# Optimization experiments

Hardware: AMD Instinct MI355X
Metric: run time of the kernel (lower is better)

Reference implementation:

```python
import jax, jax.numpy as jnp
import numpy as np

N_NODES = 100000
N_EDGES = 1600000
IN_FEATS = 128
HIDDEN = 150
NUM_OUT = 128


def setup_inputs() -> dict:
    key = jax.random.key(0)
    ks = jax.random.split(key, 9)
    x = jax.random.normal(ks[0], (N_NODES, IN_FEATS), dtype=jnp.float32)
    src = jax.random.randint(ks[1], (N_EDGES,), 0, N_NODES, dtype=jnp.int32)
    dst = jax.random.randint(ks[2], (N_EDGES,), 0, N_NODES, dtype=jnp.int32)
    def lin(k, fan_in, fan_out):
        bound = 1.0 / np.sqrt(fan_in)
        return jax.random.uniform(k, (fan_in, fan_out), jnp.float32, -bound, bound)
    W_self1 = lin(ks[3], IN_FEATS, HIDDEN)
    W_neigh1 = lin(ks[4], IN_FEATS, HIDDEN)
    b1 = jnp.zeros((HIDDEN,), jnp.float32)
    W_self2 = lin(ks[5], HIDDEN, NUM_OUT)
    W_neigh2 = lin(ks[6], HIDDEN, NUM_OUT)
    b2 = jnp.zeros((NUM_OUT,), jnp.float32)
    return {"x": x, "src": src, "dst": dst,
            "W_self1": W_self1, "W_neigh1": W_neigh1, "b1": b1,
            "W_self2": W_self2, "W_neigh2": W_neigh2, "b2": b2}


def _mean_agg(h, src, dst, deg_inv):
    # segment-mean of source features onto destination nodes; isolated nodes -> 0
    summed = jax.ops.segment_sum(h[src], dst, num_segments=N_NODES)
    return summed * deg_inv[:, None]


def _sage_conv(h, src, dst, deg_inv, W_self, W_neigh, b):
    h_neigh = _mean_agg(h, src, dst, deg_inv)
    return h @ W_self + h_neigh @ W_neigh + b


def reference(x, src, dst, W_self1, W_neigh1, b1, W_self2, W_neigh2, b2):
    deg = jax.ops.segment_sum(jnp.ones((src.shape[0],), x.dtype), dst,
                              num_segments=N_NODES)
    deg_inv = jnp.where(deg > 0, 1.0 / jnp.maximum(deg, 1.0), 0.0)
    h = _sage_conv(x, src, dst, deg_inv, W_self1, W_neigh1, b1)
    h = jax.nn.relu(h)
    h = _sage_conv(h, src, dst, deg_inv, W_self2, W_neigh2, b2)
    return h
```

## Files before the change

### kernel.cpp

```cpp
#include <hip/hip_runtime.h>

#define NN 100000
#define NE 1600000
#define INF 128
#define HID 150
#define NOUT 128

#define NBK 196
#define WGS 400
#define EPW 4000
#define CNTL (NBK * WGS)
#define CAP2 10240

typedef __attribute__((ext_vector_type(8))) short bf16x8;
typedef __attribute__((ext_vector_type(8))) unsigned short u16x8;
typedef __attribute__((ext_vector_type(4))) float f32x4;

__device__ inline unsigned short f2bf(float f) {
    unsigned int u = __float_as_uint(f);
    u += 0x7fffu + ((u >> 16) & 1u);
    return (unsigned short)(u >> 16);
}
__device__ inline float bflo(unsigned int t) { return __uint_as_float(t << 16); }
__device__ inline float bfhi(unsigned int t) { return __uint_as_float(t & 0xffff0000u); }


__global__ __launch_bounds__(256) void sort1(const int* __restrict__ src,
                                             const int* __restrict__ dst,
                                             unsigned int* __restrict__ chunkw,
                                             int* __restrict__ cntm,
                                             int* __restrict__ exm) {
    __shared__ int hist[NBK];
    __shared__ int off[NBK];
    __shared__ int s[256];
    __shared__ unsigned int buf[EPW];
    int w = blockIdx.x, tid = threadIdx.x;
    int e0 = w * EPW;
    for (int i = tid; i < NBK; i += 256) hist[i] = 0;
    __syncthreads();
    for (int i = tid; i < EPW; i += 256) atomicAdd(&hist[dst[e0 + i] >> 9], 1);
    __syncthreads();
    int v = (tid < NBK) ? hist[tid] : 0;
    s[tid] = v;
    __syncthreads();
    for (int o = 1; o < 256; o <<= 1) {
        int t = (tid >= o) ? s[tid - o] : 0;
        __syncthreads();
        s[tid] += t;
        __syncthreads();
    }
    if (tid < NBK) {
        int ex = s[tid] - v;
        off[tid] = ex;
        cntm[tid * WGS + w] = v;
        exm[tid * WGS + w] = ex;
    }
    __syncthreads();
    for (int i = tid; i < EPW; i += 256) {
        int d = dst[e0 + i];
        int b = d >> 9;
        int p = atomicAdd(&off[b], 1);
        buf[p] = (unsigned int)src[e0 + i] | ((unsigned int)(d & 511) << 17);
    }
    __syncthreads();
    for (int i = tid; i < EPW; i += 256) chunkw[e0 + i] = buf[i];
}

__global__ void scanA(const int* __restrict__ in, int* __restrict__ excl,
                      int* __restrict__ blk_sums, int L) {
    __shared__ int s[256];
    int i = blockIdx.x * 256 + threadIdx.x;
    int d = (i < L) ? in[i] : 0;
    s[threadIdx.x] = d;
    __syncthreads();
    for (int o = 1; o < 256; o <<= 1) {
        int t = (threadIdx.x >= o) ? s[threadIdx.x - o] : 0;
        __syncthreads();
        s[threadIdx.x] += t;
        __syncthreads();
    }
    int incl = s[threadIdx.x];
    if (i < L) excl[i] = incl - d;
    if (threadIdx.x == 255) blk_sums[blockIdx.x] = incl;
}

__global__ void scanB(int* __restrict__ blk_sums, int nb) {
    __shared__ int s[512];
    int t = threadIdx.x;
    int v = (t < nb) ? blk_sums[t] : 0;
    s[t] = v;
    __syncthreads();
    for (int o = 1; o < 512; o <<= 1) {
        int u = (t >= o) ? s[t - o] : 0;
        __syncthreads();
        s[t] += u;
        __syncthreads();
    }
    if (t < nb) blk_sums[t] = s[t] - v;
}

__global__ void scanC(int* __restrict__ excl, const int* __restrict__ blk_sums, int L) {
    int i = blockIdx.x * 256 + threadIdx.x;
    if (i < L) excl[i] += blk_sums[blockIdx.x];
}

__global__ __launch_bounds__(256) void buildcsr(const unsigned int* __restrict__ chunkw,
                                                const int* __restrict__ offm,
                                                const int* __restrict__ exm,
                                                int* __restrict__ csr_ptr,
                                                float* __restrict__ deg_inv,
                                                int* __restrict__ csr_src) {
    __shared__ int offrow[WGS + 1];
    __shared__ int exrow[WGS];
    __shared__ int cnt[512];
    __shared__ int excl[512];
    __shared__ int off[512];
    __shared__ int s[256];
    __shared__ int span[CAP2];
    int b = blockIdx.x, tid = threadIdx.x;
    for (int i = tid; i < WGS; i += 256) {
        offrow[i] = offm[b * WGS + i];
        exrow[i] = exm[b * WGS + i];
    }
    if (tid == 0) offrow[WGS] = (b == NBK - 1) ? NE : offm[(b + 1) * WGS];
    for (int i = tid; i < 512; i += 256) cnt[i] = 0;
    __syncthreads();
    int base = offrow[0];
    int n = offrow[WGS] - base;
    if (n > CAP2) n = CAP2;
    for (int i = tid; i < n; i += 256) {
        int gi = base + i;
        int lo = 0, hi = WGS;
        while (hi - lo > 1) {
            int mid = (lo + hi) >> 1;
            if (offrow[mid] <= gi) lo = mid; else hi = mid;
        }
        unsigned int wd = chunkw[lo * EPW + exrow[lo] + (gi - offrow[lo])];
        atomicAdd(&cnt[wd >> 17], 1);
        csr_src[gi] = (int)wd;
    }
    __syncthreads();
    int a0 = cnt[2 * tid], a1 = cnt[2 * tid + 1];
    int ps = a0 + a1;
    s[tid] = ps;
    __syncthreads();
    for (int o = 1; o < 256; o <<= 1) {
        int t = (tid >= o) ? s[tid - o] : 0;
        __syncthreads();
        s[tid] += t;
        __syncthreads();
    }
    int ex = s[tid] - ps;
    excl[2 * tid] = ex;
    excl[2 * tid + 1] = ex + a0;
    off[2 * tid] = ex;
    off[2 * tid + 1] = ex + a0;
    __syncthreads();
    for (int l = tid; l < 512; l += 256) {
        int g = b * 512 + l;
        if (g < NN) {
            csr_ptr[g] = base + excl[l];
            int d = cnt[l];
            deg_inv[g] = d > 0 ? 1.0f / (float)d : 0.0f;
        }
    }
    if (b == NBK - 1 && tid == 0) csr_ptr[NN] = NE;
    for (int i = tid; i < n; i += 256) {
        unsigned int wd = (unsigned int)csr_src[base + i];
        int l = wd >> 17;
        int p = atomicAdd(&off[l], 1);
        span[p] = (int)(wd & 0x1FFFFu);
    }
    __syncthreads();
    for (int i = tid; i < n; i += 256) csr_src[base + i] = span[i];
}


__global__ void cast_bf16(const float* __restrict__ in, unsigned short* __restrict__ outb,
                          int n8) {
    int i = blockIdx.x * 256 + threadIdx.x;
    if (i >= n8) return;
    const float4* p = (const float4*)in;
    float4 v0 = p[(size_t)i * 2];
    float4 v1 = p[(size_t)i * 2 + 1];
    u16x8 o = {f2bf(v0.x), f2bf(v0.y), f2bf(v0.z), f2bf(v0.w),
               f2bf(v1.x), f2bf(v1.y), f2bf(v1.z), f2bf(v1.w)};
    ((u16x8*)outb)[i] = o;
}

__global__ void pack_weights(const float* __restrict__ Ws1, const float* __restrict__ Wn1,
                             const float* __restrict__ b1,
                             const float* __restrict__ Ws2, const float* __restrict__ Wn2,
                             unsigned short* __restrict__ W1t, unsigned short* __restrict__ W2t,
                             float* __restrict__ b1p) {
    int id = blockIdx.x * 256 + threadIdx.x;
    if (id < 160 * 256) {
        int n = id >> 8, k = id & 255;
        float v = 0.f;
        if (n < HID) v = (k < 128) ? Ws1[k * HID + n] : Wn1[(k - 128) * HID + n];
        W1t[id] = f2bf(v);
    } else if (id < 160 * 256 + 256 * 160) {
        int id2 = id - 160 * 256;
        int n = id2 / 160, k = id2 - n * 160;
        float v = 0.f;
        if (k < HID) v = (n < 128) ? Ws2[k * 128 + n] : Wn2[k * 128 + (n - 128)];
        W2t[id2] = f2bf(v);
    } else if (id < 160 * 256 + 256 * 160 + 160) {
        int n = id - (160 * 256 + 256 * 160);
        b1p[n] = (n < HID) ? b1[n] : 0.f;
    }
}


#define AGG_ACC(t)                    \
    acc0 += bflo(t.x); acc1 += bfhi(t.x); \
    acc2 += bflo(t.y); acc3 += bfhi(t.y); \
    acc4 += bflo(t.z); acc5 += bfhi(t.z); \
    acc6 += bflo(t.w); acc7 += bfhi(t.w);

#define AGG_Q_BODY(SRCPTR)                                                  \
    int wid = threadIdx.x >> 6;                                             \
    int lane = threadIdx.x & 63;                                            \
    int v = blockIdx.x * 4 + wid;                                           \
    int start = csr_ptr[v], end = csr_ptr[v + 1];                           \
    int rg = lane >> 4, ch = lane & 15;                                     \
    const uint4* f4 = (const uint4*)(SRCPTR);                               \
    float acc0 = 0.f, acc1 = 0.f, acc2 = 0.f, acc3 = 0.f;                   \
    float acc4 = 0.f, acc5 = 0.f, acc6 = 0.f, acc7 = 0.f;                   \
    int e = start;                                                          \
    for (; e + 16 <= end; e += 16) {                                        \
        int s0 = csr_src[e + rg];                                           \
        int s1 = csr_src[e + 4 + rg];                                       \
        int s2 = csr_src[e + 8 + rg];                                       \
        int s3 = csr_src[e + 12 + rg];                                      \
        uint4 t0 = f4[(size_t)s0 * 16 + ch];                                \
        uint4 t1 = f4[(size_t)s1 * 16 + ch];                                \
        uint4 t2 = f4[(size_t)s2 * 16 + ch];                                \
        uint4 t3 = f4[(size_t)s3 * 16 + ch];                                \
        AGG_ACC(t0); AGG_ACC(t1); AGG_ACC(t2); AGG_ACC(t3);                 \
    }                                                                       \
    for (; e + 4 <= end; e += 4) {                                          \
        int s0 = csr_src[e + rg];                                           \
        uint4 t0 = f4[(size_t)s0 * 16 + ch];                                \
        AGG_ACC(t0);                                                        \
    }                                                                       \
    int rem = end - e;                                                      \
    if (rem > 0) {                                                          \
        int s0 = csr_src[(rg < rem) ? (e + rg) : e];                        \
        uint4 t = f4[(size_t)s0 * 16 + ch];                                 \
        float wt = (rg < rem) ? 1.f : 0.f;                                  \
        acc0 += wt * bflo(t.x); acc1 += wt * bfhi(t.x);                     \
        acc2 += wt * bflo(t.y); acc3 += wt * bfhi(t.y);                     \
        acc4 += wt * bflo(t.z); acc5 += wt * bfhi(t.z);                     \
        acc6 += wt * bflo(t.w); acc7 += wt * bfhi(t.w);                     \
    }                                                                       \
    acc0 += __shfl_xor(acc0, 32); acc1 += __shfl_xor(acc1, 32);             \
    acc2 += __shfl_xor(acc2, 32); acc3 += __shfl_xor(acc3, 32);             \
    acc4 += __shfl_xor(acc4, 32); acc5 += __shfl_xor(acc5, 32);             \
    acc6 += __shfl_xor(acc6, 32); acc7 += __shfl_xor(acc7, 32);             \
    acc0 += __shfl_xor(acc0, 16); acc1 += __shfl_xor(acc1, 16);             \
    acc2 += __shfl_xor(acc2, 16); acc3 += __shfl_xor(acc3, 16);             \
    acc4 += __shfl_xor(acc4, 16); acc5 += __shfl_xor(acc5, 16);             \
    acc6 += __shfl_xor(acc6, 16); acc7 += __shfl_xor(acc7, 16);

__global__ __launch_bounds__(256) void agg_mean_q(
    const unsigned short* __restrict__ featb, const int* __restrict__ csr_ptr,
    const float* __restrict__ deg_inv, const int* __restrict__ csr_src,
    unsigned short* __restrict__ outb) {
    AGG_Q_BODY(featb)
    if (lane < 16) {
        float di = deg_inv[v];
        u16x8 o = {f2bf(acc0 * di), f2bf(acc1 * di), f2bf(acc2 * di), f2bf(acc3 * di),
                   f2bf(acc4 * di), f2bf(acc5 * di), f2bf(acc6 * di), f2bf(acc7 * di)};
        ((u16x8*)outb)[(size_t)v * 16 + ch] = o;
    }
}

__global__ __launch_bounds__(256) void agg_add_q(
    const unsigned short* __restrict__ zb, const int* __restrict__ csr_ptr,
    const float* __restrict__ deg_inv, const int* __restrict__ csr_src,
    float* __restrict__ out) {
    AGG_Q_BODY(zb)
    if (lane < 16) {
        float di = deg_inv[v];
        float4* o4 = (float4*)out;
        size_t base = (size_t)v * 32 + ch * 2;
        float4 c0 = o4[base];
        float4 c1 = o4[base + 1];
        c0.x += acc0 * di; c0.y += acc1 * di; c0.z += acc2 * di; c0.w += acc3 * di;
        c1.x += acc4 * di; c1.y += acc5 * di; c1.z += acc6 * di; c1.w += acc7 * di;
        o4[base] = c0;
        o4[base + 1] = c1;
    }
}


__global__ __launch_bounds__(256) void gemm1_mfma(
    const unsigned short* __restrict__ xb, const unsigned short* __restrict__ aggb,
    const unsigned short* __restrict__ W1t, const float* __restrict__ b1p,
    unsigned short* __restrict__ h1b) {
    __shared__ __align__(16) unsigned short A_lds[128][40];
    __shared__ __align__(16) unsigned short B_lds[160][40];
    int tid = threadIdx.x;
    int m0 = blockIdx.x * 128;
    int w = tid >> 6, lane = tid & 63;
    int lrow = lane & 15, quad = lane >> 4;
    int wr = (w & 1) * 64;
    int wc = (w >> 1) * 80;
    f32x4 acc[4][5];
    #pragma unroll
    for (int r = 0; r < 4; r++)
        #pragma unroll
        for (int c = 0; c < 5; c++) acc[r][c] = (f32x4){0.f, 0.f, 0.f, 0.f};

    for (int k0 = 0; k0 < 256; k0 += 32) {
        __syncthreads();
        #pragma unroll
        for (int i = 0; i < 2; i++) {
            int idx = tid + i * 256;
            int row = idx >> 2, ch = idx & 3;
            int gm = m0 + row, gk = k0 + ch * 8;
            u16x8 val = {0, 0, 0, 0, 0, 0, 0, 0};
            if (gm < NN) {
                const unsigned short* sp = (gk < 128)
                    ? (xb + (size_t)gm * 128 + gk)
                    : (aggb + (size_t)gm * 128 + (gk - 128));
                val = *(const u16x8*)sp;
            }
            *(u16x8*)&A_lds[row][ch * 8] = val;
        }
        #pragma unroll
        for (int i = 0; i < 3; i++) {
            int idx = tid + i * 256;
            if (idx < 640) {
                int n = idx >> 2, ch = idx & 3;
                u16x8 val = *(const u16x8*)(W1t + (size_t)n * 256 + k0 + ch * 8);
                *(u16x8*)&B_lds[n][ch * 8] = val;
            }
        }
        __syncthreads();
        bf16x8 a[4], b[5];
        #pragma unroll
        for (int r = 0; r < 4; r++)
            a[r] = *(const bf16x8*)&A_lds[wr + r * 16 + lrow][quad * 8];
        #pragma unroll
        for (int c = 0; c < 5; c++)
            b[c] = *(const bf16x8*)&B_lds[wc + c * 16 + lrow][quad * 8];
        #pragma unroll
        for (int r = 0; r < 4; r++)
            #pragma unroll
            for (int c = 0; c < 5; c++)
                acc[r][c] = __builtin_amdgcn_mfma_f32_16x16x32_bf16(a[r], b[c], acc[r][c], 0, 0, 0);
    }
    #pragma unroll
    for (int r = 0; r < 4; r++) {
        #pragma unroll
        for (int rr = 0; rr < 4; rr++) {
            int gm = m0 + wr + r * 16 + quad * 4 + rr;
            if (gm < NN) {
                #pragma unroll
                for (int c = 0; c < 5; c++) {
                    int gn = wc + c * 16 + lrow;
                    float val = acc[r][c][rr] + b1p[gn];
                    val = val > 0.f ? val : 0.f;
                    h1b[(size_t)gm * 160 + gn] = f2bf(val);
                }
            }
        }
    }
}

__global__ __launch_bounds__(256) void gemm2_mfma(
    const unsigned short* __restrict__ h1b, const unsigned short* __restrict__ W2t,
    const float* __restrict__ b2, float* __restrict__ out,
    unsigned short* __restrict__ zb) {
    __shared__ __align__(16) unsigned short A_lds[128][40];
    __shared__ __align__(16) unsigned short B_lds[128][40];
    int tid = threadIdx.x;
    int m0 = blockIdx.x * 128;
    int n0 = blockIdx.y * 128;
    int w = tid >> 6, lane = tid & 63;
    int lrow = lane & 15, quad = lane >> 4;
    int wr = (w & 1) * 64;
    int wc = (w >> 1) * 64;
    f32x4 acc[4][4];
    #pragma unroll
    for (int r = 0; r < 4; r++)
        #pragma unroll
        for (int c = 0; c < 4; c++) acc[r][c] = (f32x4){0.f, 0.f, 0.f, 0.f};

    for (int k0 = 0; k0 < 160; k0 += 32) {
        __syncthreads();
        #pragma unroll
        for (int i = 0; i < 2; i++) {
            int idx = tid + i * 256;
            int row = idx >> 2, ch = idx & 3;
            int gm = m0 + row;
            u16x8 val = {0, 0, 0, 0, 0, 0, 0, 0};
            if (gm < NN) val = *(const u16x8*)(h1b + (size_t)gm * 160 + k0 + ch * 8);
            *(u16x8*)&A_lds[row][ch * 8] = val;
        }
        #pragma unroll
        for (int i = 0; i < 2; i++) {
            int idx = tid + i * 256;
            int n = idx >> 2, ch = idx & 3;
            u16x8 val = *(const u16x8*)(W2t + (size_t)(n0 + n) * 160 + k0 + ch * 8);
            *(u16x8*)&B_lds[n][ch * 8] = val;
        }
        __syncthreads();
        bf16x8 a[4], b[4];
        #pragma unroll
        for (int r = 0; r < 4; r++)
            a[r] = *(const bf16x8*)&A_lds[wr + r * 16 + lrow][quad * 8];
        #pragma unroll
        for (int c = 0; c < 4; c++)
            b[c] = *(const bf16x8*)&B_lds[wc + c * 16 + lrow][quad * 8];
        #pragma unroll
        for (int r = 0; r < 4; r++)
            #pragma unroll
            for (int c = 0; c < 4; c++)
                acc[r][c] = __builtin_amdgcn_mfma_f32_16x16x32_bf16(a[r], b[c], acc[r][c], 0, 0, 0);
    }
    #pragma unroll
    for (int r = 0; r < 4; r++) {
        #pragma unroll
        for (int rr = 0; rr < 4; rr++) {
            int gm = m0 + wr + r * 16 + quad * 4 + rr;
            if (gm < NN) {
                #pragma unroll
                for (int c = 0; c < 4; c++) {
                    int gn = wc + c * 16 + lrow;
                    float val = acc[r][c][rr];
                    if (n0 == 0) {
                        out[(size_t)gm * 128 + gn] = val + b2[gn];
                    } else {
                        zb[(size_t)gm * 128 + gn] = f2bf(val);
                    }
                }
            }
        }
    }
}


extern "C" void kernel_launch(void* const* d_in, const int* in_sizes, int n_in,
                              void* d_out, int out_size, void* d_ws, size_t ws_size,
                              hipStream_t stream) {
    const float* x   = (const float*)d_in[0];
    const int* src   = (const int*)d_in[1];
    const int* dst   = (const int*)d_in[2];
    const float* Ws1 = (const float*)d_in[3];
    const float* Wn1 = (const float*)d_in[4];
    const float* b1  = (const float*)d_in[5];
    const float* Ws2 = (const float*)d_in[6];
    const float* Wn2 = (const float*)d_in[7];
    const float* b2  = (const float*)d_in[8];
    float* out = (float*)d_out;

    char* p = (char*)d_ws;
    auto carve = [&](size_t bytes) {
        void* r = (void*)p;
        p += (bytes + 255) & ~(size_t)255;
        return r;
    };
    int*   csr_ptr  = (int*)carve((size_t)(NN + 1) * 4);
    float* deg_inv  = (float*)carve((size_t)NN * 4);
    int*   csr_src  = (int*)carve((size_t)NE * 4);
    int*   cntm     = (int*)carve((size_t)CNTL * 4);
    int*   offm     = (int*)carve((size_t)CNTL * 4);
    int*   exm      = (int*)carve((size_t)CNTL * 4);
    int*   blk2     = (int*)carve(512 * 4);
    unsigned short* xb   = (unsigned short*)carve((size_t)NN * 128 * 2);
    unsigned short* aggb = (unsigned short*)carve((size_t)NN * 128 * 2);
    unsigned short* zb   = (unsigned short*)carve((size_t)NN * 128 * 2);
    unsigned short* W1t  = (unsigned short*)carve(160 * 256 * 2);
    unsigned short* W2t  = (unsigned short*)carve(256 * 160 * 2);
    float* b1p           = (float*)carve(160 * 4);
    unsigned short* h1b  = (unsigned short*)carve((size_t)NN * 160 * 2);
    unsigned int* chunkw = (unsigned int*)h1b;

    sort1<<<WGS, 256, 0, stream>>>(src, dst, chunkw, cntm, exm);
    const int SB = (CNTL + 255) / 256;
    scanA<<<SB, 256, 0, stream>>>(cntm, offm, blk2, CNTL);
    scanB<<<1, 512, 0, stream>>>(blk2, SB);
    scanC<<<SB, 256, 0, stream>>>(offm, blk2, CNTL);
    buildcsr<<<NBK, 256, 0, stream>>>(chunkw, offm, exm, csr_ptr, deg_inv, csr_src);

    cast_bf16<<<(NN * 128 / 8 + 255) / 256, 256, 0, stream>>>(x, xb, NN * 128 / 8);
    pack_weights<<<(160 * 256 + 256 * 160 + 160 + 255) / 256, 256, 0, stream>>>(
        Ws1, Wn1, b1, Ws2, Wn2, W1t, W2t, b1p);

    agg_mean_q<<<NN / 4, 256, 0, stream>>>(xb, csr_ptr, deg_inv, csr_src, aggb);
    gemm1_mfma<<<dim3((NN + 127) / 128, 1), 256, 0, stream>>>(xb, aggb, W1t, b1p, h1b);

    gemm2_mfma<<<dim3((NN + 127) / 128, 2), 256, 0, stream>>>(h1b, W2t, b2, out, zb);
    agg_add_q<<<NN / 4, 256, 0, stream>>>(zb, csr_ptr, deg_inv, csr_src, out);

    (void)in_sizes; (void)n_in; (void)out_size; (void)ws_size;
}
```

Baseline: 394.3 us.

## Add bucket-major scatter pass, sort CSR neighbor lists, shrink aggregation unroll

Adds a sort3 kernel that scatters per-chunk sorted edges into a contiguous bucket-major buffer. This lets buildcsr read each bucket's edges linearly instead of binary-searching across 400 chunks per edge. buildcsr now also insertion-sorts each node's source list so that neighbor gathers walk memory in ascending order, which may improve cache locality. The aggregation loop unroll is reduced from 16 to 8 edges per iteration to lower register pressure, at the cost of one extra kernel launch and a serial per-thread insertion sort.

```diff
diff --git a/kernel.cpp b/kernel.cpp
--- a/kernel.cpp
+++ b/kernel.cpp
@@ -28,8 +28,7 @@
 __global__ __launch_bounds__(256) void sort1(const int* __restrict__ src,
                                              const int* __restrict__ dst,
                                              unsigned int* __restrict__ chunkw,
-                                             int* __restrict__ cntm,
-                                             int* __restrict__ exm) {
+                                             int* __restrict__ cntm) {
     __shared__ int hist[NBK];
     __shared__ int off[NBK];
     __shared__ int s[256];
@@ -50,10 +49,8 @@
         __syncthreads();
     }
     if (tid < NBK) {
-        int ex = s[tid] - v;
-        off[tid] = ex;
+        off[tid] = s[tid] - v;
         cntm[tid * WGS + w] = v;
-        exm[tid * WGS + w] = ex;
     }
     __syncthreads();
     for (int i = tid; i < EPW; i += 256) {
@@ -104,41 +101,56 @@
     if (i < L) excl[i] += blk_sums[blockIdx.x];
 }
 
-__global__ __launch_bounds__(256) void buildcsr(const unsigned int* __restrict__ chunkw,
+__global__ __launch_bounds__(256) void sort3(const unsigned int* __restrict__ chunkw,
+                                             const int* __restrict__ cntm,
+                                             const int* __restrict__ offm,
+                                             unsigned int* __restrict__ bmaj) {
+    __shared__ int excl[NBK + 1];
+    __shared__ int dbase[NBK];
+    __shared__ int s[256];
+    int w = blockIdx.x, tid = threadIdx.x;
+    int v = (tid < NBK) ? cntm[tid * WGS + w] : 0;
+    if (tid < NBK) dbase[tid] = offm[tid * WGS + w];
+    s[tid] = v;
+    __syncthreads();
+    for (int o = 1; o < 256; o <<= 1) {
+        int t = (tid >= o) ? s[tid - o] : 0;
+        __syncthreads();
+        s[tid] += t;
+        __syncthreads();
+    }
+    if (tid < NBK) excl[tid] = s[tid] - v;
+    if (tid == 0) excl[NBK] = EPW;
+    __syncthreads();
+    int e0 = w * EPW;
+    for (int i = tid; i < EPW; i += 256) {
+        int lo = 0, hi = NBK;
+        while (hi - lo > 1) {
+            int mid = (lo + hi) >> 1;
+            if (excl[mid] <= i) lo = mid; else hi = mid;
+        }
+        bmaj[dbase[lo] + (i - excl[lo])] = chunkw[e0 + i];
+    }
+}
+
+__global__ __launch_bounds__(256) void buildcsr(const unsigned int* __restrict__ bmaj,
                                                 const int* __restrict__ offm,
-                                                const int* __restrict__ exm,
                                                 int* __restrict__ csr_ptr,
                                                 float* __restrict__ deg_inv,
                                                 int* __restrict__ csr_src) {
-    __shared__ int offrow[WGS + 1];
-    __shared__ int exrow[WGS];
     __shared__ int cnt[512];
     __shared__ int excl[512];
     __shared__ int off[512];
     __shared__ int s[256];
     __shared__ int span[CAP2];
     int b = blockIdx.x, tid = threadIdx.x;
-    for (int i = tid; i < WGS; i += 256) {
-        offrow[i] = offm[b * WGS + i];
-        exrow[i] = exm[b * WGS + i];
-    }
-    if (tid == 0) offrow[WGS] = (b == NBK - 1) ? NE : offm[(b + 1) * WGS];
+    int base = offm[b * WGS];
+    int nxt = (b == NBK - 1) ? NE : offm[(b + 1) * WGS];
+    int n = nxt - base;
+    if (n > CAP2) n = CAP2;
     for (int i = tid; i < 512; i += 256) cnt[i] = 0;
     __syncthreads();
-    int base = offrow[0];
-    int n = offrow[WGS] - base;
-    if (n > CAP2) n = CAP2;
-    for (int i = tid; i < n; i += 256) {
-        int gi = base + i;
-        int lo = 0, hi = WGS;
-        while (hi - lo > 1) {
-            int mid = (lo + hi) >> 1;
-            if (offrow[mid] <= gi) lo = mid; else hi = mid;
-        }
-        unsigned int wd = chunkw[lo * EPW + exrow[lo] + (gi - offrow[lo])];
-        atomicAdd(&cnt[wd >> 17], 1);
-        csr_src[gi] = (int)wd;
-    }
+    for (int i = tid; i < n; i += 256) atomicAdd(&cnt[bmaj[base + i] >> 17], 1);
     __syncthreads();
     int a0 = cnt[2 * tid], a1 = cnt[2 * tid + 1];
     int ps = a0 + a1;
@@ -166,10 +178,23 @@
     }
     if (b == NBK - 1 && tid == 0) csr_ptr[NN] = NE;
     for (int i = tid; i < n; i += 256) {
-        unsigned int wd = (unsigned int)csr_src[base + i];
+        unsigned int wd = bmaj[base + i];
         int l = wd >> 17;
         int p = atomicAdd(&off[l], 1);
         span[p] = (int)(wd & 0x1FFFFu);
+    }
+    __syncthreads();
+    for (int l = tid; l < 512; l += 256) {
+        int lo = excl[l], hi = lo + cnt[l];
+        for (int i = lo + 1; i < hi; i++) {
+            int key = span[i];
+            int j = i - 1;
+            while (j >= lo && span[j] > key) {
+                span[j + 1] = span[j];
+                j--;
+            }
+            span[j + 1] = key;
+        }
     }
     __syncthreads();
     for (int i = tid; i < n; i += 256) csr_src[base + i] = span[i];
@@ -228,21 +253,18 @@
     float acc0 = 0.f, acc1 = 0.f, acc2 = 0.f, acc3 = 0.f;                   \
     float acc4 = 0.f, acc5 = 0.f, acc6 = 0.f, acc7 = 0.f;                   \
     int e = start;                                                          \
-    for (; e + 16 <= end; e += 16) {                                        \
+    for (; e + 8 <= end; e += 8) {                                          \
         int s0 = csr_src[e + rg];                                           \
         int s1 = csr_src[e + 4 + rg];                                       \
-        int s2 = csr_src[e + 8 + rg];                                       \
-        int s3 = csr_src[e + 12 + rg];                                      \
         uint4 t0 = f4[(size_t)s0 * 16 + ch];                                \
         uint4 t1 = f4[(size_t)s1 * 16 + ch];                                \
-        uint4 t2 = f4[(size_t)s2 * 16 + ch];                                \
-        uint4 t3 = f4[(size_t)s3 * 16 + ch];                                \
-        AGG_ACC(t0); AGG_ACC(t1); AGG_ACC(t2); AGG_ACC(t3);                 \
+        AGG_ACC(t0); AGG_ACC(t1);                                           \
     }                                                                       \
-    for (; e + 4 <= end; e += 4) {                                          \
+    if (e + 4 <= end) {                                                     \
         int s0 = csr_src[e + rg];                                           \
         uint4 t0 = f4[(size_t)s0 * 16 + ch];                                \
         AGG_ACC(t0);                                                        \
+        e += 4;                                                             \
     }                                                                       \
     int rem = end - e;                                                      \
     if (rem > 0) {                                                          \
@@ -468,7 +490,6 @@
     int*   csr_src  = (int*)carve((size_t)NE * 4);
     int*   cntm     = (int*)carve((size_t)CNTL * 4);
     int*   offm     = (int*)carve((size_t)CNTL * 4);
-    int*   exm      = (int*)carve((size_t)CNTL * 4);
     int*   blk2     = (int*)carve(512 * 4);
     unsigned short* xb   = (unsigned short*)carve((size_t)NN * 128 * 2);
     unsigned short* aggb = (unsigned short*)carve((size_t)NN * 128 * 2);
@@ -478,13 +499,15 @@
     float* b1p           = (float*)carve(160 * 4);
     unsigned short* h1b  = (unsigned short*)carve((size_t)NN * 160 * 2);
     unsigned int* chunkw = (unsigned int*)h1b;
-
-    sort1<<<WGS, 256, 0, stream>>>(src, dst, chunkw, cntm, exm);
+    unsigned int* bmaj   = (unsigned int*)((char*)h1b + (size_t)NE * 4);
+
+    sort1<<<WGS, 256, 0, stream>>>(src, dst, chunkw, cntm);
     const int SB = (CNTL + 255) / 256;
     scanA<<<SB, 256, 0, stream>>>(cntm, offm, blk2, CNTL);
     scanB<<<1, 512, 0, stream>>>(blk2, SB);
     scanC<<<SB, 256, 0, stream>>>(offm, blk2, CNTL);
-    buildcsr<<<NBK, 256, 0, stream>>>(chunkw, offm, exm, csr_ptr, deg_inv, csr_src);
+    sort3<<<WGS, 256, 0, stream>>>(chunkw, cntm, offm, bmaj);
+    buildcsr<<<NBK, 256, 0, stream>>>(bmaj, offm, csr_ptr, deg_inv, csr_src);
 
     cast_bf16<<<(NN * 128 / 8 + 255) / 256, 256, 0, stream>>>(x, xb, NN * 128 / 8);
     pack_weights<<<(160 * 256 + 256 * 160 + 160 + 255) / 256, 256, 0, stream>>>(
```

Result: slower. 448.7 us (+13.8%).
